# Performance work log

Hardware: AMD Instinct MI355X
Metric: run time of the kernel (lower is better)

Reference implementation:

```python
import jax, jax.numpy as jnp
import numpy as np

ORDER = 2            # spline order kx = ky
H = W = 7            # control_grid_dims
KSZ = 3.0            # kernel_size -> bbox = (-1.5, 1.5)
OUT, IN = 32, 32     # out_channels, in_groups (groups=1)
N = 32768            # number of query points
BBOX = KSZ / 2.0


def _make_knots(n_coef, lo, hi, order):
    # clamped knot vector of length n_coef + order + 1 (as scipy produces)
    n_interior = n_coef - order - 1
    interior = np.linspace(lo, hi, n_interior + 2)[1:-1]
    t = np.concatenate([[lo] * (order + 1), interior, [hi] * (order + 1)])
    return jnp.asarray(t, dtype=jnp.float32)


def setup_inputs() -> dict:
    key = jax.random.key(0)
    k1, k2 = jax.random.split(key)
    # query points strictly inside the bbox
    xy = jax.random.uniform(k1, (N, 2), dtype=jnp.float32,
                            minval=-BBOX * 0.95, maxval=BBOX * 0.95)
    # control coefficients C: [out_channels, in_groups, h, w]
    C = jax.random.normal(k2, (OUT, IN, H, W), dtype=jnp.float32) * 0.1
    Tx = _make_knots(H, -BBOX, BBOX, ORDER)
    Ty = _make_knots(W, -BBOX, BBOX, ORDER)
    return {"xy": xy, "Tx": Tx, "Ty": Ty, "C": C}


def _find_span(T, v, p):
    # torch: (T <= v).min(dim=-1) -> first False index, minus 1; if all True -> len(T)-p-2
    ss = jnp.searchsorted(T, v, side="right")          # number of knots <= v
    return jnp.where(ss == T.shape[0], T.shape[0] - p - 2, ss - 1)


def _safe_div(num, den):
    return num / jnp.where(den == 0, jnp.ones_like(den), den)


def reference(xy, Tx, Ty, C):
    px = py = ORDER
    X = xy[:, 0]
    Y = xy[:, 1]
    kx = _find_span(Tx, X, px)   # [N] knot spans
    ky = _find_span(Ty, Y, py)

    dim = OUT * IN
    Ctrl = C.reshape(dim, H, W)
    offs = jnp.arange(px + 1)
    ix = kx[:, None] - px + offs                 # [N, px+1]
    iy = ky[:, None] - py + offs                 # [N, py+1]
    # gather local (px+1)x(py+1) control patch per point: [N, Dim, px+1, py+1]
    D = Ctrl[:, ix[:, :, None], iy[:, None, :]]
    D = jnp.transpose(D, (1, 0, 2, 3))

    rng = jnp.arange(px)
    # de Boor recursion along x
    for r in range(1, px + 1):
        t_lo = Tx[kx[:, None] - px + 1 + rng]    # [N, px]
        t_hi = Tx[kx[:, None] + 2 - r + rng]
        alphax = _safe_div(X[:, None] - t_lo, t_hi - t_lo)
        for j in range(px, r - 1, -1):
            a = alphax[:, j - 1][:, None, None]
            D = D.at[:, :, j, :].set((1 - a) * D[:, :, j - 1, :] + a * D[:, :, j, :])
    # de Boor recursion along y (on the collapsed x row px)
    for r in range(1, py + 1):
        t_lo = Ty[ky[:, None] - py + 1 + rng]
        t_hi = Ty[ky[:, None] + 2 - r + rng]
        alphay = _safe_div(Y[:, None] - t_lo, t_hi - t_lo)
        for j in range(py, r - 1, -1):
            a = alphay[:, j - 1][:, None]
            D = D.at[:, :, px, j].set((1 - a) * D[:, :, px, j - 1] + a * D[:, :, px, j])

    return D[:, :, px, py].reshape(xy.shape[0], OUT, IN)
```

## Files before the change

### kernel.cpp

```cpp
#include <hip/hip_runtime.h>


#define NPTS   32768
#define DIM    1024
#define MT     (NPTS / 16)
#define WELEM  (MT * 2 * 64 * 8)

typedef _Float16 f16x8 __attribute__((ext_vector_type(8)));
typedef float    f32x4 __attribute__((ext_vector_type(4)));

__device__ __forceinline__ float safe_div(float n, float d) {
    return (d == 0.0f) ? n : (n / d);
}

__device__ __forceinline__ void span_weights(float v, const float* __restrict__ T,
                                             int& k, float& w0, float& w1, float& w2) {
    float t3 = T[3], t4 = T[4], t5 = T[5], t6 = T[6];
    k = 2 + (v >= t3) + (v >= t4) + (v >= t5) + (v >= t6);
    float Tm1 = T[k - 1], T0 = T[k], Tp1 = T[k + 1], Tp2 = T[k + 2];
    float a10 = safe_div(v - Tm1, Tp1 - Tm1);
    float a11 = safe_div(v - T0,  Tp2 - T0);
    float a21 = safe_div(v - T0,  Tp1 - T0);
    w0 = (1.0f - a21) * (1.0f - a10);
    w1 = (1.0f - a21) * a10 + a21 * (1.0f - a11);
    w2 = a21 * a11;
}

__global__ __launch_bounds__(256) void prep_kernel(
    const float* __restrict__ xy,
    const float* __restrict__ Tx,
    const float* __restrict__ Ty,
    const float* __restrict__ C,
    _Float16* __restrict__ Wp,
    _Float16* __restrict__ Cp)
{
    const int b = blockIdx.x;
    const int t = threadIdx.x;
    if (b < MT / 2) {
        const int id   = b * 256 + t;
        const int lane = id & 63;
        const int step = (id >> 6) & 1;
        const int tile = id >> 7;
        const int n    = tile * 16 + (lane & 15);
        const int g    = lane >> 4;

        const float2 pt = ((const float2*)xy)[n];
        int kx, ky;
        float wx0, wx1, wx2, wy0, wy1, wy2;
        span_weights(pt.x, Tx, kx, wx0, wx1, wx2);
        span_weights(pt.y, Ty, ky, wy0, wy1, wy2);
        const int off = (kx - 2) * 7 + (ky - 2);

        f16x8 frag;
#pragma unroll
        for (int j = 0; j < 8; ++j) {
            const int k   = step * 32 + g * 8 + j;
            const int rel = k - off;
            const float va = (rel >= 14) ? wx2 : ((rel >= 7) ? wx1 : wx0);
            const int   bb = rel - ((rel >= 14) ? 14 : ((rel >= 7) ? 7 : 0));
            const float vb = (bb == 0) ? wy0 : ((bb == 1) ? wy1 : wy2);
            const bool valid = (rel >= 0) && (rel <= 16) && (bb >= 0) && (bb <= 2);
            frag[j] = (_Float16)(valid ? va * vb : 0.0f);
        }
        *(f16x8*)(Wp + (size_t)id * 8) = frag;
    } else if (b < MT / 2 + 32) {
        const int id    = (b - MT / 2) * 256 + t;
        const int lane  = id & 63;
        const int step  = (id >> 6) & 1;
        const int ctile = id >> 7;
        const int ch    = ctile * 16 + (lane & 15);
        const int g     = lane >> 4;

        f16x8 frag;
#pragma unroll
        for (int j = 0; j < 8; ++j) {
            const int k = step * 32 + g * 8 + j;
            frag[j] = (_Float16)((k < 49) ? C[(size_t)ch * 49 + k] : 0.0f);
        }
        *(f16x8*)(Cp + (size_t)id * 8) = frag;
    }
}

__global__ __launch_bounds__(256, 4) void spline_mfma_kernel(
    const _Float16* __restrict__ Wp,
    const _Float16* __restrict__ Cp,
    float* __restrict__ out)
{
    __shared__ float lds[2][16 * 256];

    const int t      = threadIdx.x;
    const int lane   = t & 63;
    const int w      = t >> 6;
    const int chgrp  = blockIdx.x & 3;
    const int pchunk = blockIdx.x >> 2;

    f16x8 af[4][2];
#pragma unroll
    for (int ct = 0; ct < 4; ++ct)
#pragma unroll
        for (int st = 0; st < 2; ++st) {
            const int ctg = chgrp * 16 + w * 4 + ct;
            af[ct][st] = *(const f16x8*)(Cp + ((size_t)(ctg * 2 + st) * 64 + lane) * 8);
        }

    const int p = lane & 15;
    const int h = lane >> 4;

#pragma unroll
    for (int pt = 0; pt < 8; ++pt) {
        const int ptile = pchunk * 8 + pt;
        const f16x8 b0 = *(const f16x8*)(Wp + ((size_t)(ptile * 2 + 0) * 64 + lane) * 8);
        const f16x8 b1 = *(const f16x8*)(Wp + ((size_t)(ptile * 2 + 1) * 64 + lane) * 8);

        f32x4 acc[4];
#pragma unroll
        for (int ct = 0; ct < 4; ++ct) {
            f32x4 z; z[0] = 0.0f; z[1] = 0.0f; z[2] = 0.0f; z[3] = 0.0f;
            acc[ct] = __builtin_amdgcn_mfma_f32_16x16x32_f16(af[ct][0], b0, z, 0, 0, 0);
        }
#pragma unroll
        for (int ct = 0; ct < 4; ++ct)
            acc[ct] = __builtin_amdgcn_mfma_f32_16x16x32_f16(af[ct][1], b1, acc[ct], 0, 0, 0);

        float* buf = lds[pt & 1];
#pragma unroll
        for (int ct = 0; ct < 4; ++ct) {
            const int ci = w * 64 + ct * 16 + h * 4;
            *(f32x4*)(buf + p * 256 + (ci ^ ((p & 7) << 2))) = acc[ct];
        }
        __syncthreads();

#pragma unroll
        for (int r = 0; r < 4; ++r) {
            const int pr = 4 * w + r;
            const int ci = lane * 4;
            f32x4 v = *(const f32x4*)(buf + pr * 256 + (ci ^ ((pr & 7) << 2)));
            float* dst = out + (size_t)(ptile * 16 + pr) * DIM + chgrp * 256 + ci;
            __builtin_nontemporal_store(v, (f32x4*)dst);
        }
    }
}

extern "C" void kernel_launch(void* const* d_in, const int* in_sizes, int n_in,
                              void* d_out, int out_size, void* d_ws, size_t ws_size,
                              hipStream_t stream) {
    const float* xy = (const float*)d_in[0];
    const float* Tx = (const float*)d_in[1];
    const float* Ty = (const float*)d_in[2];
    const float* C  = (const float*)d_in[3];
    float* out = (float*)d_out;

    _Float16* Wp = (_Float16*)d_ws;
    _Float16* Cp = Wp + WELEM;

    prep_kernel<<<MT / 2 + 32, 256, 0, stream>>>(xy, Tx, Ty, C, Wp, Cp);
    spline_mfma_kernel<<<4 * (MT / 8), 256, 0, stream>>>(Wp, Cp, out);
}
```

Measured before the change: 36.89 us.

## Use per-wave LDS transpose buffers and prefetch next point tile

Each wave now gets a private LDS region and transposes only its own 16x64 accumulator tile. This removes the block-wide __syncthreads between the MFMA write and the store read. The next tile's B fragments are loaded one iteration ahead to hide global load latency. Stores now cover 64 contiguous channels per row instead of 256, which may make the write pattern less coalesced. There is also no barrier between reusing the per-wave buffer across iterations, so correctness depends on in-wave ordering.

```diff
diff --git a/kernel.cpp b/kernel.cpp
--- a/kernel.cpp
+++ b/kernel.cpp
@@ -86,13 +86,15 @@
     const _Float16* __restrict__ Cp,
     float* __restrict__ out)
 {
-    __shared__ float lds[2][16 * 256];
+    __shared__ float lds[4 * 1024];
 
     const int t      = threadIdx.x;
     const int lane   = t & 63;
     const int w      = t >> 6;
     const int chgrp  = blockIdx.x & 3;
     const int pchunk = blockIdx.x >> 2;
+
+    float* const wbuf = lds + w * 1024;
 
     f16x8 af[4][2];
 #pragma unroll
@@ -105,12 +107,21 @@
 
     const int p = lane & 15;
     const int h = lane >> 4;
+    const int cb = lane & 15;
+
+    const int ptile0 = pchunk * 8;
+    f16x8 nb0 = *(const f16x8*)(Wp + ((size_t)(ptile0 * 2 + 0) * 64 + lane) * 8);
+    f16x8 nb1 = *(const f16x8*)(Wp + ((size_t)(ptile0 * 2 + 1) * 64 + lane) * 8);
 
 #pragma unroll
     for (int pt = 0; pt < 8; ++pt) {
         const int ptile = pchunk * 8 + pt;
-        const f16x8 b0 = *(const f16x8*)(Wp + ((size_t)(ptile * 2 + 0) * 64 + lane) * 8);
-        const f16x8 b1 = *(const f16x8*)(Wp + ((size_t)(ptile * 2 + 1) * 64 + lane) * 8);
+        const f16x8 b0 = nb0;
+        const f16x8 b1 = nb1;
+        if (pt + 1 < 8) {
+            nb0 = *(const f16x8*)(Wp + ((size_t)((ptile + 1) * 2 + 0) * 64 + lane) * 8);
+            nb1 = *(const f16x8*)(Wp + ((size_t)((ptile + 1) * 2 + 1) * 64 + lane) * 8);
+        }
 
         f32x4 acc[4];
 #pragma unroll
@@ -122,20 +133,20 @@
         for (int ct = 0; ct < 4; ++ct)
             acc[ct] = __builtin_amdgcn_mfma_f32_16x16x32_f16(af[ct][1], b1, acc[ct], 0, 0, 0);
 
-        float* buf = lds[pt & 1];
 #pragma unroll
         for (int ct = 0; ct < 4; ++ct) {
-            const int ci = w * 64 + ct * 16 + h * 4;
-            *(f32x4*)(buf + p * 256 + (ci ^ ((p & 7) << 2))) = acc[ct];
+            const int g16 = ct * 4 + h;
+            const int col = (g16 & 8) | ((g16 ^ p) & 7);
+            *(f32x4*)(wbuf + p * 64 + (col << 2)) = acc[ct];
         }
-        __syncthreads();
 
 #pragma unroll
-        for (int r = 0; r < 4; ++r) {
-            const int pr = 4 * w + r;
-            const int ci = lane * 4;
-            f32x4 v = *(const f32x4*)(buf + pr * 256 + (ci ^ ((pr & 7) << 2)));
-            float* dst = out + (size_t)(ptile * 16 + pr) * DIM + chgrp * 256 + ci;
+        for (int gg = 0; gg < 4; ++gg) {
+            const int pr  = gg * 4 + h;
+            const int col = (cb & 8) | ((cb ^ pr) & 7);
+            f32x4 v = *(const f32x4*)(wbuf + pr * 64 + (col << 2));
+            float* dst = out + (size_t)(ptile * 16 + pr) * DIM
+                             + chgrp * 256 + w * 64 + cb * 4;
             __builtin_nontemporal_store(v, (f32x4*)dst);
         }
     }
```

Result: no change. 37.31 us (+1.1%).
